# Kernel optimization log

Hardware: AMD Instinct MI355X
Metric: run time of the kernel (lower is better)

Reference implementation:

```python
import jax, jax.numpy as jnp
import numpy as np

L, D, B, N, E, T = 3, 64, 1024, 131072, 1048576, 16
CH, HID = L * D, (L * D) // 2  # channel_dim=192, reduction=2 -> 96
BN_EPS = 1e-5


def setup_inputs() -> dict:
    key = jax.random.key(0)
    ks = jax.random.split(key, 20)
    rn = lambda k, sh, s=0.1: jax.random.normal(k, sh, jnp.float32) * s
    return {
        "query_x": rn(ks[0], (N, D), 1.0),
        "corpus_x": rn(ks[1], (N, D), 1.0),
        "query_edge_index": jax.random.randint(ks[2], (2, E), 0, N),
        "corpus_edge_index": jax.random.randint(ks[3], (2, E), 0, N),
        "query_graph_idx": jnp.sort(jax.random.randint(ks[4], (N,), 0, B)),
        "corpus_graph_idx": jnp.sort(jax.random.randint(ks[5], (N,), 0, B)),
        "gin_w1": rn(ks[6], (L, D, D)),
        "gin_b1": jnp.zeros((L, D), jnp.float32),
        "gin_w2": rn(ks[7], (L, D, D)),
        "gin_b2": jnp.zeros((L, D), jnp.float32),
        "bn_gamma": jnp.ones((L, D), jnp.float32),
        "bn_beta": jnp.zeros((L, D), jnp.float32),
        "gin_eps": jnp.zeros((L,), jnp.float32),
        "inner_w": rn(ks[8], (L, D, D)),
        "inner_b": jnp.zeros((L, D), jnp.float32),
        "outer_w": rn(ks[9], (L, D, D)),
        "outer_b": jnp.zeros((L, D), jnp.float32),
        "conv_w1": rn(ks[10], (CH, HID)),
        "conv_b1": jnp.zeros((HID,), jnp.float32),
        "conv_w2": rn(ks[11], (HID, HID)),
        "conv_b2": jnp.zeros((HID,), jnp.float32),
        "score_w1": rn(ks[12], (HID, 16)),
        "score_b1": jnp.zeros((16,), jnp.float32),
        "score_w2": rn(ks[13], (16, 1)),
        "score_b2": jnp.zeros((1,), jnp.float32),
        "ntn_w": rn(ks[14], (D, D, T), 0.05),
        "ntn_wb": rn(ks[15], (T, 2 * D), 0.05),
        "ntn_bias": jnp.zeros((T,), jnp.float32),
        "sim_w1": rn(ks[16], (T, T)),
        "sim_b1": jnp.zeros((T,), jnp.float32),
        "sim_w2": rn(ks[17], (T, 1)),
        "sim_b2": jnp.zeros((1,), jnp.float32),
        "alpha": jnp.ones((1,), jnp.float32),
        "beta": jnp.ones((1,), jnp.float32),
    }


def _encode(x, edge_index, graph_idx, p):
    """EncodingLayer: per layer GINConv -> ReLU -> inner MLP -> segment-sum pool -> outer MLP."""
    src, dst = edge_index[0], edge_index[1]
    feats = []
    for i in range(L):
        agg = jax.ops.segment_sum(x[src], dst, num_segments=N)  # neighbor sum (gather->scatter)
        h = (1.0 + p["gin_eps"][i]) * x + agg                    # GIN aggregation
        h = jax.nn.relu(h @ p["gin_w1"][i] + p["gin_b1"][i]) @ p["gin_w2"][i] + p["gin_b2"][i]
        mu = h.mean(axis=0)
        var = h.var(axis=0)
        h = (h - mu) * jax.lax.rsqrt(var + BN_EPS) * p["bn_gamma"][i] + p["bn_beta"][i]  # BatchNorm1d (train stats)
        x = jax.nn.relu(h)
        inner = jax.nn.relu(x @ p["inner_w"][i] + p["inner_b"][i])
        pooled = jax.ops.segment_sum(inner, graph_idx, num_segments=B)  # [B, D] graph pooling
        feats.append(jax.nn.relu(pooled @ p["outer_w"][i] + p["outer_b"][i]))
    return jnp.concatenate(feats, axis=1)  # [B, L*D]


def reference(query_x, corpus_x, query_edge_index, corpus_edge_index, query_graph_idx, corpus_graph_idx, gin_w1, gin_b1, gin_w2, gin_b2, bn_gamma, bn_beta, gin_eps, inner_w, inner_b, outer_w, outer_b, conv_w1, conv_b1, conv_w2, conv_b2, score_w1, score_b1, score_w2, score_b2, ntn_w, ntn_wb, ntn_bias, sim_w1, sim_b1, sim_w2, sim_b2, alpha, beta):
    p = {"gin_w1": gin_w1, "gin_b1": gin_b1, "gin_w2": gin_w2, "gin_b2": gin_b2,
         "bn_gamma": bn_gamma, "bn_beta": bn_beta, "gin_eps": gin_eps,
         "inner_w": inner_w, "inner_b": inner_b, "outer_w": outer_w, "outer_b": outer_b}
    qf = _encode(query_x, query_edge_index, query_graph_idx, p)   # [B, CH]
    cf = _encode(corpus_x, corpus_edge_index, corpus_graph_idx, p)
    # diff branch: conv_stack + score_layer
    diff = jnp.exp(-jnp.square(qf - cf))
    h = jax.nn.relu(diff @ conv_w1 + conv_b1)
    h = jnp.tanh(h @ conv_w2 + conv_b2)
    score = jax.nn.sigmoid(jax.nn.relu(h @ score_w1 + score_b1) @ score_w2 + score_b2)[:, 0]
    # NTN interaction branch on last-layer (filters[-1]) graph embeddings
    e1, e2 = qf[:, -D:], cf[:, -D:]
    scoring = jnp.einsum('bf,fgt,bg->bt', e1, ntn_w, e2)
    block = jnp.concatenate([e1, e2], axis=1) @ ntn_wb.T
    sim_rep = jax.nn.relu(scoring + block + ntn_bias)
    sim = jax.nn.sigmoid(jax.nn.relu(sim_rep @ sim_w1 + sim_b1) @ sim_w2 + sim_b2)[:, 0]
    return alpha[0] * score + beta[0] * sim  # [B]
```

## Files before the change

kernel.cpp:

```cpp
#include <hip/hip_runtime.h>
#include <hip/hip_bf16.h>

typedef __hip_bfloat16 bf16;
typedef __attribute__((ext_vector_type(8))) short short8;
typedef __attribute__((ext_vector_type(4))) float floatx4;

#define NN     131072
#define NEDGE  1048576
#define BG     1024
#define LAYERS 3
#define TG     8

__device__ __forceinline__ short f2bf_s(float f){
    union { float f; unsigned u; } x; x.f = f;
    unsigned r = x.u + 0x7fffu + ((x.u >> 16) & 1u);
    return (short)(r >> 16);
}
__device__ __forceinline__ float bf2f_s(short s){
    union { unsigned u; float f; } x; x.u = ((unsigned)(unsigned short)s) << 16;
    return x.f;
}
__device__ __forceinline__ void acc4(const unsigned short* p,
                                     float& a0, float& a1, float& a2, float& a3){
    ushort4 u = *(const ushort4*)p;
    a0 += bf2f_s((short)u.x); a1 += bf2f_s((short)u.y);
    a2 += bf2f_s((short)u.z); a3 += bf2f_s((short)u.w);
}

__global__ __launch_bounds__(256) void k_offsets(const int* __restrict__ gi,
                                                 int* __restrict__ off)
{
    int g = blockIdx.x*256 + threadIdx.x;
    if (g > BG) return;
    int lo = 0, hi = NN;
    while (lo < hi) { int mid = (lo + hi) >> 1; if (gi[mid] < g) lo = mid + 1; else hi = mid; }
    off[g] = lo;
}

__global__ __launch_bounds__(256) void k_zero(int* __restrict__ cnt)
{
    int i = blockIdx.x*256 + threadIdx.x;
    if (i < NN) cnt[i] = 0;
}

__global__ __launch_bounds__(256) void k_hist(const int* __restrict__ ei,
                                              int* __restrict__ cnt,
                                              int* __restrict__ rank)
{
    int e = blockIdx.x*256 + threadIdx.x;
    rank[e] = atomicAdd(cnt + ei[NEDGE + e], 1);
}

__global__ __launch_bounds__(256) void k_scan1(const int* __restrict__ cnt,
    int* __restrict__ rowptr, int* __restrict__ bsum)
{
    __shared__ int sd[256];
    int t = threadIdx.x;
    int base = blockIdx.x*1024 + t*4;
    int c0 = cnt[base], c1 = cnt[base+1], c2 = cnt[base+2], c3 = cnt[base+3];
    int tsum = c0 + c1 + c2 + c3;
    sd[t] = tsum;
    __syncthreads();
    for (int off = 1; off < 256; off <<= 1) {
        int v = (t >= off) ? sd[t-off] : 0;
        __syncthreads();
        sd[t] += v;
        __syncthreads();
    }
    int excl = sd[t] - tsum;
    rowptr[base]   = excl;
    rowptr[base+1] = excl + c0;
    rowptr[base+2] = excl + c0 + c1;
    rowptr[base+3] = excl + c0 + c1 + c2;
    if (t == 255) bsum[blockIdx.x] = sd[255];
}

__global__ __launch_bounds__(128) void k_scan2(const int* __restrict__ bsum,
    int* __restrict__ boff, int* __restrict__ rowptr)
{
    __shared__ int sd[128];
    int t = threadIdx.x;
    int v0 = bsum[t];
    sd[t] = v0;
    __syncthreads();
    for (int off = 1; off < 128; off <<= 1) {
        int v = (t >= off) ? sd[t-off] : 0;
        __syncthreads();
        sd[t] += v;
        __syncthreads();
    }
    boff[t] = sd[t] - v0;
    if (t == 0) rowptr[NN] = NEDGE;
}

__global__ __launch_bounds__(256) void k_scan3(int* __restrict__ rowptr,
    const int* __restrict__ boff)
{
    int i = blockIdx.x*256 + threadIdx.x;
    rowptr[i] += boff[i >> 10];
}

__global__ __launch_bounds__(256) void k_fill(const int* __restrict__ ei,
    const int* __restrict__ rowptr, const int* __restrict__ rank,
    int* __restrict__ col)
{
    int e = blockIdx.x*256 + threadIdx.x;
    int s = ei[e];
    int d = ei[NEDGE + e];
    col[rowptr[d] + rank[e]] = s;
}

__global__ __launch_bounds__(256) void k_cvt(const float* __restrict__ x,
                                             bf16* __restrict__ xh,
                                             float* __restrict__ stats)
{
    int i = blockIdx.x*256 + threadIdx.x;
    xh[i] = __float2bfloat16(x[i]);
    if (blockIdx.x == 0 && threadIdx.x < 128) stats[threadIdx.x] = 0.f;
}

__global__ __launch_bounds__(256) void k_wprep(
    const float* __restrict__ gw1, const float* __restrict__ gw2,
    const float* __restrict__ iw,
    short* __restrict__ w1h, short* __restrict__ w1l,
    short* __restrict__ w2h, short* __restrict__ w2l,
    short* __restrict__ wih, short* __restrict__ wil)
{
    int i = blockIdx.x*256 + threadIdx.x;
    if (i >= 3*LAYERS*4096) return;
    int msel = i / (LAYERS*4096);
    int rem  = i % (LAYERS*4096);
    int l = rem >> 12, idx = rem & 4095;
    int n = idx >> 6, k = idx & 63;
    const float* src = (msel==0) ? gw1 : (msel==1) ? gw2 : iw;
    float v = src[l*4096 + k*64 + n];
    short hi = f2bf_s(v);
    short lo = f2bf_s(v - bf2f_s(hi));
    short* dh = (msel==0) ? w1h : (msel==1) ? w2h : wih;
    short* dl = (msel==0) ? w1l : (msel==1) ? w2l : wil;
    dh[rem] = hi;
    dl[rem] = lo;
}

__global__ __launch_bounds__(256) void k_agg_gin(
    const bf16* __restrict__ xh,
    const int* __restrict__ rowptr, const int* __restrict__ col,
    const float* __restrict__ epsp,
    const short* __restrict__ w1h, const short* __restrict__ w1l,
    const float* __restrict__ b1,
    const short* __restrict__ w2h, const short* __restrict__ w2l,
    const float* __restrict__ b2,
    float* __restrict__ big, float* __restrict__ stats)
{
    __shared__ __align__(16) char buf[4][9472];
    __shared__ float red[2][4][64];
    int tid = threadIdx.x, wv = tid >> 6, lane = tid & 63;
    int q = lane >> 4, m = lane & 15;
    int nb = blockIdx.x*128 + wv*32;
    short* Sh = (short*)buf[wv];
    short* Sl = Sh + 2304;
    float ep = 1.0f + *epsp;

    int gv = rowptr[nb + (lane < 33 ? lane : 32)];
    int grp = q;
    int fo = m * 4;
    const unsigned short* xt = (const unsigned short*)xh;

    for (int i = 0; i < 8; i++) {
        int row = i*4 + grp;
        int rs = __shfl(gv, row, 64);
        int re = __shfl(gv, row+1, 64);
        float a0=0.f,a1=0.f,a2=0.f,a3=0.f;
        float e0=0.f,e1=0.f,e2=0.f,e3=0.f;
        float g0=0.f,g1=0.f,g2=0.f,g3=0.f;
        float h0=0.f,h1=0.f,h2=0.f,h3=0.f;
        int r = rs;
        for (; r + 4 <= re; r += 4) {
            int ca = col[r], cb = col[r+1], cc = col[r+2], cd = col[r+3];
            acc4(xt + (((size_t)ca) << 6) + fo, a0,a1,a2,a3);
            acc4(xt + (((size_t)cb) << 6) + fo, e0,e1,e2,e3);
            acc4(xt + (((size_t)cc) << 6) + fo, g0,g1,g2,g3);
            acc4(xt + (((size_t)cd) << 6) + fo, h0,h1,h2,h3);
        }
        for (; r < re; r++)
            acc4(xt + (((size_t)col[r]) << 6) + fo, a0,a1,a2,a3);
        a0 += e0 + g0 + h0;
        a1 += e1 + g1 + h1;
        a2 += e2 + g2 + h2;
        a3 += e3 + g3 + h3;
        ushort4 sv = *(const ushort4*)(xt + (((size_t)(nb+row)) << 6) + fo);
        a0 = fmaf(ep, bf2f_s((short)sv.x), a0);
        a1 = fmaf(ep, bf2f_s((short)sv.y), a1);
        a2 = fmaf(ep, bf2f_s((short)sv.z), a2);
        a3 = fmaf(ep, bf2f_s((short)sv.w), a3);
        short4 hh, ll;
        hh.x = f2bf_s(a0); ll.x = f2bf_s(a0 - bf2f_s(hh.x));
        hh.y = f2bf_s(a1); ll.y = f2bf_s(a1 - bf2f_s(hh.y));
        hh.z = f2bf_s(a2); ll.z = f2bf_s(a2 - bf2f_s(hh.z));
        hh.w = f2bf_s(a3); ll.w = f2bf_s(a3 - bf2f_s(hh.w));
        *(short4*)(Sh + row*72 + fo) = hh;
        *(short4*)(Sl + row*72 + fo) = ll;
    }
    __syncthreads();

    short8 Ah[2][2], Al[2][2];
    #pragma unroll
    for (int mc=0; mc<2; mc++)
      #pragma unroll
      for (int kc=0; kc<2; kc++){
        Ah[mc][kc] = *(const short8*)(Sh + (mc*16+m)*72 + kc*32 + q*8);
        Al[mc][kc] = *(const short8*)(Sl + (mc*16+m)*72 + kc*32 + q*8);
      }
    floatx4 acc[2][4];
    #pragma unroll
    for (int mc=0;mc<2;mc++)
      #pragma unroll
      for (int nc=0;nc<4;nc++) acc[mc][nc] = (floatx4){0.f,0.f,0.f,0.f};
    #pragma unroll
    for (int nc=0;nc<4;nc++){
      #pragma unroll
      for (int kc=0;kc<2;kc++){
        short8 bh = *(const short8*)(w1h + (nc*16+m)*64 + kc*32 + q*8);
        short8 bl = *(const short8*)(w1l + (nc*16+m)*64 + kc*32 + q*8);
        #pragma unroll
        for (int mc=0;mc<2;mc++){
          acc[mc][nc] = __builtin_amdgcn_mfma_f32_16x16x32_bf16(Ah[mc][kc], bh, acc[mc][nc],0,0,0);
          acc[mc][nc] = __builtin_amdgcn_mfma_f32_16x16x32_bf16(Al[mc][kc], bh, acc[mc][nc],0,0,0);
          acc[mc][nc] = __builtin_amdgcn_mfma_f32_16x16x32_bf16(Ah[mc][kc], bl, acc[mc][nc],0,0,0);
        }
      }
    }

    #pragma unroll
    for (int nc=0;nc<4;nc++){
      float bia = b1[nc*16+m];
      #pragma unroll
      for (int mc=0;mc<2;mc++)
        #pragma unroll
        for (int r=0;r<4;r++){
          float v = fmaxf(acc[mc][nc][r] + bia, 0.f);
          int row = mc*16 + q*4 + r, cl = nc*16 + m;
          short hb = f2bf_s(v);
          Sh[row*72+cl] = hb;
          Sl[row*72+cl] = f2bf_s(v - bf2f_s(hb));
        }
    }
    __syncthreads();

    short8 A2h[2][2], A2l[2][2];
    #pragma unroll
    for (int mc=0; mc<2; mc++)
      #pragma unroll
      for (int kc=0; kc<2; kc++){
        A2h[mc][kc] = *(const short8*)(Sh + (mc*16+m)*72 + kc*32 + q*8);
        A2l[mc][kc] = *(const short8*)(Sl + (mc*16+m)*72 + kc*32 + q*8);
      }
    floatx4 acc2[2][4];
    #pragma unroll
    for (int mc=0;mc<2;mc++)
      #pragma unroll
      for (int nc=0;nc<4;nc++) acc2[mc][nc] = (floatx4){0.f,0.f,0.f,0.f};
    #pragma unroll
    for (int nc=0;nc<4;nc++){
      #pragma unroll
      for (int kc=0;kc<2;kc++){
        short8 bh = *(const short8*)(w2h + (nc*16+m)*64 + kc*32 + q*8);
        short8 bl = *(const short8*)(w2l + (nc*16+m)*64 + kc*32 + q*8);
        #pragma unroll
        for (int mc=0;mc<2;mc++){
          acc2[mc][nc] = __builtin_amdgcn_mfma_f32_16x16x32_bf16(A2h[mc][kc], bh, acc2[mc][nc],0,0,0);
          acc2[mc][nc] = __builtin_amdgcn_mfma_f32_16x16x32_bf16(A2l[mc][kc], bh, acc2[mc][nc],0,0,0);
          acc2[mc][nc] = __builtin_amdgcn_mfma_f32_16x16x32_bf16(A2h[mc][kc], bl, acc2[mc][nc],0,0,0);
        }
      }
    }

    #pragma unroll
    for (int nc=0;nc<4;nc++){
      float bia = b2[nc*16+m];
      float s = 0.f, s2 = 0.f;
      #pragma unroll
      for (int mc=0;mc<2;mc++)
        #pragma unroll
        for (int r=0;r<4;r++){
          float v = acc2[mc][nc][r] + bia;
          big[(((size_t)(nb + mc*16 + q*4 + r)) << 6) + nc*16 + m] = v;
          s += v; s2 = fmaf(v, v, s2);
        }
      s  += __shfl_xor(s, 16, 64);  s  += __shfl_xor(s, 32, 64);
      s2 += __shfl_xor(s2,16, 64);  s2 += __shfl_xor(s2,32, 64);
      if (q == 0){ red[0][wv][nc*16+m] = s; red[1][wv][nc*16+m] = s2; }
    }
    __syncthreads();
    if (tid < 128){
      int which = tid >> 6, c = tid & 63;
      float a = red[which][0][c]+red[which][1][c]+red[which][2][c]+red[which][3][c];
      unsafeAtomicAdd(stats + which*64 + c, a);
    }
}

__global__ __launch_bounds__(64) void k_bnfin(float* __restrict__ stats,
                        const float* __restrict__ gamma,
                        const float* __restrict__ beta,
                        float* __restrict__ bnp,
                        float* __restrict__ pooled)
{
    if (blockIdx.x == 0) {
        int c = threadIdx.x;
        float mu  = stats[c]     * (1.0f/NN);
        float ex2 = stats[64+c]  * (1.0f/NN);
        float var = ex2 - mu*mu;
        float sc  = gamma[c] * rsqrtf(var + 1e-5f);
        bnp[c]     = sc;
        bnp[64+c]  = beta[c] - mu*sc;
        stats[c] = 0.f; stats[64+c] = 0.f;
    } else {
        int base = (blockIdx.x - 1)*256 + threadIdx.x;
        #pragma unroll
        for (int i = 0; i < 4; i++) pooled[base + i*64] = 0.f;
    }
}

__global__ __launch_bounds__(256) void k_bn_inner(
    const float* __restrict__ big, const float* __restrict__ bnp,
    const short* __restrict__ wih, const short* __restrict__ wil,
    const float* __restrict__ bi,
    bf16* __restrict__ xh,
    const int* __restrict__ gidx, float* __restrict__ pooled)
{
    __shared__ __align__(16) char buf[4][9472];
    int tid = threadIdx.x, wv = tid >> 6, lane = tid & 63;
    int q = lane >> 4, m = lane & 15;
    int nb = blockIdx.x*128 + wv*32;
    short* Sh = (short*)buf[wv];
    short* Sl = Sh + 2304;

    float sc = bnp[lane], sh = bnp[64 + lane];
    for (int rr = 0; rr < 32; rr++){
        float v = big[(((size_t)(nb+rr)) << 6) + lane];
        v = fmaxf(fmaf(v, sc, sh), 0.f);
        xh[(((size_t)(nb+rr)) << 6) + lane] = __float2bfloat16(v);
        short hb = f2bf_s(v);
        Sh[rr*72 + lane] = hb;
        Sl[rr*72 + lane] = f2bf_s(v - bf2f_s(hb));
    }
    __syncthreads();

    short8 A2h[2][2], A2l[2][2];
    #pragma unroll
    for (int mc=0; mc<2; mc++)
      #pragma unroll
      for (int kc=0; kc<2; kc++){
        A2h[mc][kc] = *(const short8*)(Sh + (mc*16+m)*72 + kc*32 + q*8);
        A2l[mc][kc] = *(const short8*)(Sl + (mc*16+m)*72 + kc*32 + q*8);
      }
    floatx4 acc[2][4];
    #pragma unroll
    for (int mc=0;mc<2;mc++)
      #pragma unroll
      for (int nc=0;nc<4;nc++) acc[mc][nc] = (floatx4){0.f,0.f,0.f,0.f};
    #pragma unroll
    for (int nc=0;nc<4;nc++){
      #pragma unroll
      for (int kc=0;kc<2;kc++){
        short8 bh = *(const short8*)(wih + (nc*16+m)*64 + kc*32 + q*8);
        short8 bl = *(const short8*)(wil + (nc*16+m)*64 + kc*32 + q*8);
        #pragma unroll
        for (int mc=0;mc<2;mc++){
          acc[mc][nc] = __builtin_amdgcn_mfma_f32_16x16x32_bf16(A2h[mc][kc], bh, acc[mc][nc],0,0,0);
          acc[mc][nc] = __builtin_amdgcn_mfma_f32_16x16x32_bf16(A2l[mc][kc], bh, acc[mc][nc],0,0,0);
          acc[mc][nc] = __builtin_amdgcn_mfma_f32_16x16x32_bf16(A2h[mc][kc], bl, acc[mc][nc],0,0,0);
        }
      }
    }
    __syncthreads();

    float* P = (float*)buf[wv];
    #pragma unroll
    for (int nc=0;nc<4;nc++){
      float bia = bi[nc*16+m];
      #pragma unroll
      for (int mc=0;mc<2;mc++)
        #pragma unroll
        for (int r=0;r<4;r++){
          float v = fmaxf(acc[mc][nc][r] + bia, 0.f);
          P[(mc*16 + q*4 + r)*66 + nc*16 + m] = v;
        }
    }
    __syncthreads();

    int gv = (lane < 32) ? gidx[nb + lane] : 0;
    int cur = __shfl(gv, 0, 64);
    float a = 0.f;
    for (int rr = 0; rr < 32; rr++){
        int g = __shfl(gv, rr, 64);
        if (g != cur){
            unsafeAtomicAdd(pooled + (size_t)cur*64 + lane, a);
            a = 0.f; cur = g;
        }
        a += P[rr*66 + lane];
    }
    unsafeAtomicAdd(pooled + (size_t)cur*64 + lane, a);
}

__global__ __launch_bounds__(256) void k_outer(const float* __restrict__ pooled,
    const float* __restrict__ w, const float* __restrict__ b,
    float* __restrict__ feats, int coff)
{
    int g = blockIdx.x*256 + threadIdx.x;
    int bb = g >> 6, j = g & 63;
    const float* pr = pooled + bb*64;
    float a = b[j];
    for (int k = 0; k < 64; k++) a = fmaf(pr[k], w[k*64 + j], a);
    feats[bb*192 + coff + j] = fmaxf(a, 0.f);
}

__global__ __launch_bounds__(256) void k_tail(
    const float* __restrict__ qf, const float* __restrict__ cf,
    const float* __restrict__ cw1, const float* __restrict__ cb1,
    const float* __restrict__ cw2, const float* __restrict__ cb2,
    const float* __restrict__ sw1, const float* __restrict__ sb1,
    const float* __restrict__ sw2, const float* __restrict__ sb2,
    const float* __restrict__ nw,  const float* __restrict__ nwb,
    const float* __restrict__ nb,
    const float* __restrict__ mw1, const float* __restrict__ mb1,
    const float* __restrict__ mw2, const float* __restrict__ mb2,
    const float* __restrict__ alpha, const float* __restrict__ beta,
    float* __restrict__ out)
{
    __shared__ float cws[192*96];
    __shared__ float diff[TG][192];
    __shared__ float e1s[TG][64], e2s[TG][64];
    __shared__ float h1s[TG][96], h2s[TG][96];
    __shared__ float s1s[TG][16], s2s[TG][16], srep[TG][16];
    __shared__ float red[16][16][TG];

    int t = threadIdx.x;
    int b0 = blockIdx.x * TG;

    for (int i = t; i < 192*96; i += 256) cws[i] = cw1[i];
    for (int i = t; i < TG*192; i += 256) {
        int b = i / 192, f = i % 192;
        float qv = qf[(b0+b)*192 + f], cv = cf[(b0+b)*192 + f];
        float d = qv - cv;
        diff[b][f] = __expf(-d*d);
        if (f >= 128) { e1s[b][f-128] = qv; e2s[b][f-128] = cv; }
    }
    __syncthreads();

    {
        int b = t >> 5, o = (t & 31) * 3;
        float a0 = cb1[o], a1 = cb1[o+1], a2 = cb1[o+2];
        for (int f = 0; f < 192; f++) {
            float d = diff[b][f];
            const float* w = cws + f*96 + o;
            a0 = fmaf(d, w[0], a0);
            a1 = fmaf(d, w[1], a1);
            a2 = fmaf(d, w[2], a2);
        }
        h1s[b][o] = fmaxf(a0, 0.f);
        h1s[b][o+1] = fmaxf(a1, 0.f);
        h1s[b][o+2] = fmaxf(a2, 0.f);
    }
    __syncthreads();
    for (int i = t; i < 96*96; i += 256) cws[i] = cw2[i];
    __syncthreads();
    {
        int b = t >> 5, o = (t & 31) * 3;
        float a0 = cb2[o], a1 = cb2[o+1], a2 = cb2[o+2];
        for (int f = 0; f < 96; f++) {
            float d = h1s[b][f];
            const float* w = cws + f*96 + o;
            a0 = fmaf(d, w[0], a0);
            a1 = fmaf(d, w[1], a1);
            a2 = fmaf(d, w[2], a2);
        }
        h2s[b][o] = tanhf(a0);
        h2s[b][o+1] = tanhf(a1);
        h2s[b][o+2] = tanhf(a2);
    }
    __syncthreads();
    if (t < TG*16) {
        int b = t >> 4, o = t & 15;
        float a = sb1[o];
        for (int f = 0; f < 96; f++) a = fmaf(h2s[b][f], sw1[f*16+o], a);
        s1s[b][o] = fmaxf(a, 0.f);
    }

    {
        int tt = t & 15, gq = t >> 4;
        int g0 = gq * 4;
        int lane = t & 63;
        float e1v[TG];
        #pragma unroll
        for (int b = 0; b < TG; b++) e1v[b] = e1s[b][lane];
        float v0[TG], v1[TG], v2[TG], v3[TG];
        #pragma unroll
        for (int b = 0; b < TG; b++) { v0[b]=0.f; v1[b]=0.f; v2[b]=0.f; v3[b]=0.f; }
        for (int f = 0; f < 64; f++) {
            const float* wp = nw + ((size_t)f*64 + g0)*16 + tt;
            float w0 = wp[0], w1 = wp[16], w2 = wp[32], w3 = wp[48];
            #pragma unroll
            for (int b = 0; b < TG; b++) {
                float e = __shfl(e1v[b], f, 64);
                v0[b] = fmaf(e, w0, v0[b]);
                v1[b] = fmaf(e, w1, v1[b]);
                v2[b] = fmaf(e, w2, v2[b]);
                v3[b] = fmaf(e, w3, v3[b]);
            }
        }
        #pragma unroll
        for (int b = 0; b < TG; b++) {
            float p = v0[b]*e2s[b][g0] + v1[b]*e2s[b][g0+1]
                    + v2[b]*e2s[b][g0+2] + v3[b]*e2s[b][g0+3];
            red[gq][tt][b] = p;
        }
    }
    __syncthreads();
    if (t < TG*16) {
        int b = t >> 4, tt = t & 15;
        float scv = 0.f;
        #pragma unroll
        for (int gq = 0; gq < 16; gq++) scv += red[gq][tt][b];
        float blk = nb[tt];
        for (int f = 0; f < 64; f++) blk = fmaf(e1s[b][f], nwb[tt*128 + f], blk);
        for (int f = 0; f < 64; f++) blk = fmaf(e2s[b][f], nwb[tt*128 + 64 + f], blk);
        srep[b][tt] = fmaxf(scv + blk, 0.f);
    }
    __syncthreads();
    if (t < TG*16) {
        int b = t >> 4, o = t & 15;
        float a = mb1[o];
        #pragma unroll
        for (int f = 0; f < 16; f++) a = fmaf(srep[b][f], mw1[f*16+o], a);
        s2s[b][o] = fmaxf(a, 0.f);
    }
    __syncthreads();
    if (t < TG) {
        float sco = sb2[0], sm = mb2[0];
        #pragma unroll
        for (int f = 0; f < 16; f++) {
            sco = fmaf(s1s[t][f], sw2[f], sco);
            sm  = fmaf(s2s[t][f], mw2[f], sm);
        }
        float score = 1.f / (1.f + __expf(-sco));
        float sim   = 1.f / (1.f + __expf(-sm));
        out[b0 + t] = alpha[0]*score + beta[0]*sim;
    }
}

extern "C" void kernel_launch(void* const* d_in, const int* in_sizes, int n_in,
                              void* d_out, int out_size, void* d_ws, size_t ws_size,
                              hipStream_t stream)
{
    const float* qx  = (const float*)d_in[0];
    const float* cx  = (const float*)d_in[1];
    const int*   qei = (const int*)d_in[2];
    const int*   cei = (const int*)d_in[3];
    const int*   qgi = (const int*)d_in[4];
    const int*   cgi = (const int*)d_in[5];
    const float* Wgw1 = (const float*)d_in[6];
    const float* Wgb1 = (const float*)d_in[7];
    const float* Wgw2 = (const float*)d_in[8];
    const float* Wgb2 = (const float*)d_in[9];
    const float* Wgam = (const float*)d_in[10];
    const float* Wbet = (const float*)d_in[11];
    const float* Weps = (const float*)d_in[12];
    const float* Wiw  = (const float*)d_in[13];
    const float* Wib  = (const float*)d_in[14];
    const float* Wow  = (const float*)d_in[15];
    const float* Wob  = (const float*)d_in[16];
    const float* Wcw1 = (const float*)d_in[17];
    const float* Wcb1 = (const float*)d_in[18];
    const float* Wcw2 = (const float*)d_in[19];
    const float* Wcb2 = (const float*)d_in[20];
    const float* Wsw1 = (const float*)d_in[21];
    const float* Wsb1 = (const float*)d_in[22];
    const float* Wsw2 = (const float*)d_in[23];
    const float* Wsb2 = (const float*)d_in[24];
    const float* Wnw  = (const float*)d_in[25];
    const float* Wnwb = (const float*)d_in[26];
    const float* Wnb  = (const float*)d_in[27];
    const float* Wmw1 = (const float*)d_in[28];
    const float* Wmb1 = (const float*)d_in[29];
    const float* Wmw2 = (const float*)d_in[30];
    const float* Wmb2 = (const float*)d_in[31];
    const float* Wal  = (const float*)d_in[32];
    const float* Wbe  = (const float*)d_in[33];

    float* F      = (float*)d_ws;
    float* big    = F;
    float* stats  = F + 8388608;
    float* bnp    = stats + 128;
    float* pooled = bnp + 128;
    float* qf     = pooled + 65536;
    float* cf     = qf + 196608;
    int*   qoff   = (int*)(cf + 196608);
    int*   coff   = qoff + (BG + 1);
    int*   rowptr = coff + (BG + 1);
    int*   cnt    = rowptr + (NN + 1);
    int*   col    = cnt + NN;
    int*   bsum   = col + NEDGE;
    int*   boff   = bsum + 128;
    bf16*  xh     = (bf16*)(boff + 128);
    int*   rank   = (int*)big;
    uintptr_t wtb = (uintptr_t)(xh + (size_t)NN*64);
    wtb = (wtb + 63) & ~((uintptr_t)63);
    short* w1h = (short*)wtb;
    short* w1l = w1h + 3*4096;
    short* w2h = w1l + 3*4096;
    short* w2l = w2h + 3*4096;
    short* wih = w2l + 3*4096;
    short* wil = wih + 3*4096;

    k_wprep<<<144, 256, 0, stream>>>(Wgw1, Wgw2, Wiw, w1h, w1l, w2h, w2l, wih, wil);

    for (int side = 0; side < 2; side++) {
        const float* x0 = side ? cx  : qx;
        const int* ei   = side ? cei : qei;
        const int* gi   = side ? cgi : qgi;
        int* off        = side ? coff : qoff;
        float* feats    = side ? cf  : qf;

        k_offsets<<<5, 256, 0, stream>>>(gi, off);

        k_zero<<<NN/256, 256, 0, stream>>>(cnt);
        k_hist<<<NEDGE/256, 256, 0, stream>>>(ei, cnt, rank);
        k_scan1<<<128, 256, 0, stream>>>(cnt, rowptr, bsum);
        k_scan2<<<1, 128, 0, stream>>>(bsum, boff, rowptr);
        k_scan3<<<NN/256, 256, 0, stream>>>(rowptr, boff);
        k_fill<<<NEDGE/256, 256, 0, stream>>>(ei, rowptr, rank, col);

        k_cvt<<<NN*64/256, 256, 0, stream>>>(x0, xh, stats);

        for (int l = 0; l < LAYERS; l++) {
            k_agg_gin<<<NN/128, 256, 0, stream>>>(xh, rowptr, col, Weps + l,
                                                  w1h + l*4096, w1l + l*4096, Wgb1 + l*64,
                                                  w2h + l*4096, w2l + l*4096, Wgb2 + l*64,
                                                  big, stats);
            k_bnfin<<<257, 64, 0, stream>>>(stats, Wgam + l*64, Wbet + l*64, bnp, pooled);
            k_bn_inner<<<NN/128, 256, 0, stream>>>(big, bnp,
                                                   wih + l*4096, wil + l*4096,
                                                   Wib + l*64, xh, gi, pooled);
            k_outer<<<BG*64/256, 256, 0, stream>>>(pooled, Wow + l*4096, Wob + l*64,
                                                   feats, l*64);
        }
    }

    k_tail<<<BG/TG, 256, 0, stream>>>(qf, cf, Wcw1, Wcb1, Wcw2, Wcb2,
                                      Wsw1, Wsb1, Wsw2, Wsb2,
                                      Wnw, Wnwb, Wnb, Wmw1, Wmb1, Wmw2, Wmb2,
                                      Wal, Wbe, (float*)d_out);
}
```

Baseline: 976.4 us.

## Fold BN finalize and outer MLP into neighboring kernels, drop small launches

Removes the k_offsets, k_bnfin and k_outer launches. BN scale and shift are now computed inline in k_bn_inner from per-layer stats buffers. Each layer's outer MLP is deferred into the next k_agg_gin, into k_zero for the last query layer, and into k_tail for the last corpus layer. Pooled and stats buffers are made per-layer and zeroed once in a vectorized k_cvt. This cuts about 12 small launches and their serialization gaps, at the cost of extra work in a few blocks of the larger kernels and more scratch memory.

Result: faster. 922.6 us (-5.5%).

```diff
diff --git a/kernel.cpp b/kernel.cpp
--- a/kernel.cpp
+++ b/kernel.cpp
@@ -27,20 +27,19 @@
     a2 += bf2f_s((short)u.z); a3 += bf2f_s((short)u.w);
 }
 
-__global__ __launch_bounds__(256) void k_offsets(const int* __restrict__ gi,
-                                                 int* __restrict__ off)
-{
-    int g = blockIdx.x*256 + threadIdx.x;
-    if (g > BG) return;
-    int lo = 0, hi = NN;
-    while (lo < hi) { int mid = (lo + hi) >> 1; if (gi[mid] < g) lo = mid + 1; else hi = mid; }
-    off[g] = lo;
-}
-
-__global__ __launch_bounds__(256) void k_zero(int* __restrict__ cnt)
+__global__ __launch_bounds__(256) void k_zero(int* __restrict__ cnt,
+    const float* __restrict__ pooled_prev, const float* __restrict__ owp,
+    const float* __restrict__ obp, float* __restrict__ feats_prev)
 {
     int i = blockIdx.x*256 + threadIdx.x;
     if (i < NN) cnt[i] = 0;
+    if (pooled_prev && blockIdx.x < 256) {
+        int bb = i >> 6, j = i & 63;
+        const float* pr = pooled_prev + bb*64;
+        float a = obp[j];
+        for (int k = 0; k < 64; k++) a = fmaf(pr[k], owp[k*64 + j], a);
+        feats_prev[bb*192 + 128 + j] = fmaxf(a, 0.f);
+    }
 }
 
 __global__ __launch_bounds__(256) void k_hist(const int* __restrict__ ei,
@@ -112,11 +111,15 @@
 
 __global__ __launch_bounds__(256) void k_cvt(const float* __restrict__ x,
                                              bf16* __restrict__ xh,
-                                             float* __restrict__ stats)
+                                             float* __restrict__ zbuf)
 {
     int i = blockIdx.x*256 + threadIdx.x;
-    xh[i] = __float2bfloat16(x[i]);
-    if (blockIdx.x == 0 && threadIdx.x < 128) stats[threadIdx.x] = 0.f;
+    float4 v = ((const float4*)x)[i];
+    short4 o;
+    o.x = f2bf_s(v.x); o.y = f2bf_s(v.y);
+    o.z = f2bf_s(v.z); o.w = f2bf_s(v.w);
+    ((short4*)xh)[i] = o;
+    if (i < 3*128 + 3*BG*64) zbuf[i] = 0.f;
 }
 
 __global__ __launch_bounds__(256) void k_wprep(
@@ -150,7 +153,9 @@
     const float* __restrict__ b1,
     const short* __restrict__ w2h, const short* __restrict__ w2l,
     const float* __restrict__ b2,
-    float* __restrict__ big, float* __restrict__ stats)
+    float* __restrict__ big, float* __restrict__ stats,
+    const float* __restrict__ pooled_prev, const float* __restrict__ owp,
+    const float* __restrict__ obp, float* __restrict__ feats, int coffp)
 {
     __shared__ __align__(16) char buf[4][9472];
     __shared__ float red[2][4][64];
@@ -161,13 +166,21 @@
     short* Sl = Sh + 2304;
     float ep = 1.0f + *epsp;
 
+    if (pooled_prev && blockIdx.x < 256) {
+        int g = blockIdx.x*256 + tid;
+        int bb = g >> 6, j = g & 63;
+        const float* pr = pooled_prev + bb*64;
+        float a = obp[j];
+        for (int k = 0; k < 64; k++) a = fmaf(pr[k], owp[k*64 + j], a);
+        feats[bb*192 + coffp + j] = fmaxf(a, 0.f);
+    }
+
     int gv = rowptr[nb + (lane < 33 ? lane : 32)];
-    int grp = q;
     int fo = m * 4;
     const unsigned short* xt = (const unsigned short*)xh;
 
     for (int i = 0; i < 8; i++) {
-        int row = i*4 + grp;
+        int row = i*4 + q;
         int rs = __shfl(gv, row, 64);
         int re = __shfl(gv, row+1, 64);
         float a0=0.f,a1=0.f,a2=0.f,a3=0.f;
@@ -299,30 +312,9 @@
     }
 }
 
-__global__ __launch_bounds__(64) void k_bnfin(float* __restrict__ stats,
-                        const float* __restrict__ gamma,
-                        const float* __restrict__ beta,
-                        float* __restrict__ bnp,
-                        float* __restrict__ pooled)
-{
-    if (blockIdx.x == 0) {
-        int c = threadIdx.x;
-        float mu  = stats[c]     * (1.0f/NN);
-        float ex2 = stats[64+c]  * (1.0f/NN);
-        float var = ex2 - mu*mu;
-        float sc  = gamma[c] * rsqrtf(var + 1e-5f);
-        bnp[c]     = sc;
-        bnp[64+c]  = beta[c] - mu*sc;
-        stats[c] = 0.f; stats[64+c] = 0.f;
-    } else {
-        int base = (blockIdx.x - 1)*256 + threadIdx.x;
-        #pragma unroll
-        for (int i = 0; i < 4; i++) pooled[base + i*64] = 0.f;
-    }
-}
-
 __global__ __launch_bounds__(256) void k_bn_inner(
-    const float* __restrict__ big, const float* __restrict__ bnp,
+    const float* __restrict__ big, const float* __restrict__ stats,
+    const float* __restrict__ gam, const float* __restrict__ bet,
     const short* __restrict__ wih, const short* __restrict__ wil,
     const float* __restrict__ bi,
     bf16* __restrict__ xh,
@@ -335,7 +327,12 @@
     short* Sh = (short*)buf[wv];
     short* Sl = Sh + 2304;
 
-    float sc = bnp[lane], sh = bnp[64 + lane];
+    float mu  = stats[lane]    * (1.0f/NN);
+    float ex2 = stats[64+lane] * (1.0f/NN);
+    float var = ex2 - mu*mu;
+    float sc  = gam[lane] * rsqrtf(var + 1e-5f);
+    float sh  = bet[lane] - mu*sc;
+
     for (int rr = 0; rr < 32; rr++){
         float v = big[(((size_t)(nb+rr)) << 6) + lane];
         v = fmaxf(fmaf(v, sc, sh), 0.f);
@@ -403,20 +400,10 @@
     unsafeAtomicAdd(pooled + (size_t)cur*64 + lane, a);
 }
 
-__global__ __launch_bounds__(256) void k_outer(const float* __restrict__ pooled,
-    const float* __restrict__ w, const float* __restrict__ b,
-    float* __restrict__ feats, int coff)
-{
-    int g = blockIdx.x*256 + threadIdx.x;
-    int bb = g >> 6, j = g & 63;
-    const float* pr = pooled + bb*64;
-    float a = b[j];
-    for (int k = 0; k < 64; k++) a = fmaf(pr[k], w[k*64 + j], a);
-    feats[bb*192 + coff + j] = fmaxf(a, 0.f);
-}
-
 __global__ __launch_bounds__(256) void k_tail(
     const float* __restrict__ qf, const float* __restrict__ cf,
+    const float* __restrict__ pooled_c2,
+    const float* __restrict__ ow2, const float* __restrict__ ob2,
     const float* __restrict__ cw1, const float* __restrict__ cb1,
     const float* __restrict__ cw2, const float* __restrict__ cb2,
     const float* __restrict__ sw1, const float* __restrict__ sb1,
@@ -438,13 +425,28 @@
     int t = threadIdx.x;
     int b0 = blockIdx.x * TG;
 
+    {
+        int b = t >> 5, o = (t & 31) * 2;
+        const float* pr = pooled_c2 + (size_t)(b0 + b)*64;
+        float a0 = ob2[o], a1 = ob2[o+1];
+        for (int k = 0; k < 64; k++) {
+            float p = pr[k];
+            a0 = fmaf(p, ow2[k*64 + o], a0);
+            a1 = fmaf(p, ow2[k*64 + o + 1], a1);
+        }
+        e2s[b][o]   = fmaxf(a0, 0.f);
+        e2s[b][o+1] = fmaxf(a1, 0.f);
+    }
     for (int i = t; i < 192*96; i += 256) cws[i] = cw1[i];
+    __syncthreads();
+
     for (int i = t; i < TG*192; i += 256) {
         int b = i / 192, f = i % 192;
-        float qv = qf[(b0+b)*192 + f], cv = cf[(b0+b)*192 + f];
+        float qv = qf[(b0+b)*192 + f];
+        float cv = (f < 128) ? cf[(b0+b)*192 + f] : e2s[b][f-128];
         float d = qv - cv;
         diff[b][f] = __expf(-d*d);
-        if (f >= 128) { e1s[b][f-128] = qv; e2s[b][f-128] = cv; }
+        if (f >= 128) e1s[b][f-128] = qv;
     }
     __syncthreads();
 
@@ -590,14 +592,12 @@
 
     float* F      = (float*)d_ws;
     float* big    = F;
-    float* stats  = F + 8388608;
-    float* bnp    = stats + 128;
-    float* pooled = bnp + 128;
-    float* qf     = pooled + 65536;
+    float* zbuf   = F + 8388608;
+    float* stats3 = zbuf;
+    float* pooled3= zbuf + 384;
+    float* qf     = pooled3 + 3*BG*64;
     float* cf     = qf + 196608;
-    int*   qoff   = (int*)(cf + 196608);
-    int*   coff   = qoff + (BG + 1);
-    int*   rowptr = coff + (BG + 1);
+    int*   rowptr = (int*)(cf + 196608);
     int*   cnt    = rowptr + (NN + 1);
     int*   col    = cnt + NN;
     int*   bsum   = col + NEDGE;
@@ -619,35 +619,41 @@
         const float* x0 = side ? cx  : qx;
         const int* ei   = side ? cei : qei;
         const int* gi   = side ? cgi : qgi;
-        int* off        = side ? coff : qoff;
         float* feats    = side ? cf  : qf;
 
-        k_offsets<<<5, 256, 0, stream>>>(gi, off);
-
-        k_zero<<<NN/256, 256, 0, stream>>>(cnt);
+        if (side == 0)
+            k_zero<<<NN/256, 256, 0, stream>>>(cnt, nullptr, nullptr, nullptr, nullptr);
+        else
+            k_zero<<<NN/256, 256, 0, stream>>>(cnt, pooled3 + 2*BG*64,
+                                               Wow + 2*4096, Wob + 2*64, qf);
         k_hist<<<NEDGE/256, 256, 0, stream>>>(ei, cnt, rank);
         k_scan1<<<128, 256, 0, stream>>>(cnt, rowptr, bsum);
         k_scan2<<<1, 128, 0, stream>>>(bsum, boff, rowptr);
         k_scan3<<<NN/256, 256, 0, stream>>>(rowptr, boff);
         k_fill<<<NEDGE/256, 256, 0, stream>>>(ei, rowptr, rank, col);
 
-        k_cvt<<<NN*64/256, 256, 0, stream>>>(x0, xh, stats);
+        k_cvt<<<NN*64/1024, 256, 0, stream>>>(x0, xh, zbuf);
 
         for (int l = 0; l < LAYERS; l++) {
+            const float* pprev = (l == 0) ? nullptr : pooled3 + (size_t)(l-1)*BG*64;
+            const float* owp   = (l == 0) ? nullptr : Wow + (l-1)*4096;
+            const float* obp   = (l == 0) ? nullptr : Wob + (l-1)*64;
             k_agg_gin<<<NN/128, 256, 0, stream>>>(xh, rowptr, col, Weps + l,
                                                   w1h + l*4096, w1l + l*4096, Wgb1 + l*64,
                                                   w2h + l*4096, w2l + l*4096, Wgb2 + l*64,
-                                                  big, stats);
-            k_bnfin<<<257, 64, 0, stream>>>(stats, Wgam + l*64, Wbet + l*64, bnp, pooled);
-            k_bn_inner<<<NN/128, 256, 0, stream>>>(big, bnp,
+                                                  big, stats3 + l*128,
+                                                  pprev, owp, obp, feats, (l-1)*64);
+            k_bn_inner<<<NN/128, 256, 0, stream>>>(big, stats3 + l*128,
+                                                   Wgam + l*64, Wbet + l*64,
                                                    wih + l*4096, wil + l*4096,
-                                                   Wib + l*64, xh, gi, pooled);
-            k_outer<<<BG*64/256, 256, 0, stream>>>(pooled, Wow + l*4096, Wob + l*64,
-                                                   feats, l*64);
-        }
-    }
-
-    k_tail<<<BG/TG, 256, 0, stream>>>(qf, cf, Wcw1, Wcb1, Wcw2, Wcb2,
+                                                   Wib + l*64, xh, gi,
+                                                   pooled3 + (size_t)l*BG*64);
+        }
+    }
+
+    k_tail<<<BG/TG, 256, 0, stream>>>(qf, cf, pooled3 + 2*BG*64,
+                                      Wow + 2*4096, Wob + 2*64,
+                                      Wcw1, Wcb1, Wcw2, Wcb2,
                                       Wsw1, Wsb1, Wsw2, Wsb2,
                                       Wnw, Wnwb, Wnb, Wmw1, Wmb1, Wmw2, Wmb2,
                                       Wal, Wbe, (float*)d_out);
```
